# Kernel optimization log

Measured on AMD Instinct MI355X. Metric: run time of the kernel, lower is better.

## Reference

```python
import jax, jax.numpy as jnp
import numpy as np

B, N = 64, 1500
F_MIN, F_MAX = 0.5, 3.0  # HR band in Hz (30-180 bpm)
SAMPLING_F = 0.002       # frequency grid step -> F = 1251 frequencies
FS = 30.0                # video frame rate


def setup_inputs() -> dict:
    key = jax.random.key(0)
    k1, k2 = jax.random.split(key)
    x = jax.random.normal(k1, (B, N), dtype=jnp.float32)
    # true frequencies inside the searched band
    f_true = jax.random.uniform(k2, (B,), dtype=jnp.float32, minval=F_MIN, maxval=F_MAX)
    fs = jnp.full((B,), FS, dtype=jnp.float32)
    deltas = jnp.zeros((B,), dtype=jnp.float32)  # accepted but unused by the loss
    return {
        "x": x,
        "f_true": f_true,
        "fs": fs,
        "deltas": deltas,
        "sampling_f": SAMPLING_F,
        "f_range": (F_MIN, F_MAX),
    }


def reference(x, f_true, fs, deltas, sampling_f, f_range):
    f_min, f_max = f_range
    # frequency grid, same semantics as torch.arange(f_min, f_max+step, step)
    f_values = jnp.arange(f_min, f_max + sampling_f, sampling_f, dtype=jnp.float32)  # [F]
    n = jnp.arange(x.shape[1], dtype=jnp.float32)  # [N] time indices
    # angles[b,f,n] = 2*pi * f_values[f] * n / fs[b]  (fs varies per sample)
    phase = (2.0 * jnp.pi) * (f_values[None, :, None] * n[None, None, :]) / fs[:, None, None]  # [B,F,N]
    # PSD at each grid frequency: (sum x cos)^2 + (sum x sin)^2, batched as one contraction
    cos_terms = jnp.einsum('bn,bfn->bf', x, jnp.cos(phase))  # [B,F]
    sin_terms = jnp.einsum('bn,bfn->bf', x, jnp.sin(phase))  # [B,F]
    psd = cos_terms ** 2 + sin_terms ** 2                    # [B,F]
    log_lik = jnp.log(jax.nn.softmax(psd, axis=1) + 1e-8)    # [B,F]
    # index of grid frequency closest to f_true (non-differentiable gather index)
    idx = jnp.argmin(jnp.abs(f_values[None, :] - f_true[:, None]), axis=1)  # [B]
    per_sample = -jnp.take_along_axis(log_lik, idx[:, None], axis=1)[:, 0]  # [B]
    return jnp.mean(per_sample)
```

## Files before the change

### kernel.cpp

```cpp
#include <hip/hip_runtime.h>

#define BATCH 64
#define NSAMP 1500
#define NFREQ 1251
#define NSEG  5
#define SEGLEN 300
#define FBLK  256
#define FCHUNKS 5


#define CTRL_CNT    0
#define CTRL_GCNT   64
#define CTRL_PROBE  128
#define CTRL_PIDX   256
#define CTRL_LVAL   320
#define CTRL_STATS  384

__device__ __forceinline__ unsigned rmw_read32(unsigned* p) {
    return __hip_atomic_fetch_add(p, 0u, __ATOMIC_RELAXED, __HIP_MEMORY_SCOPE_AGENT);
}
__device__ __forceinline__ unsigned long long rmw_read64(unsigned long long* p) {
    return __hip_atomic_fetch_add(p, 0ull, __ATOMIC_RELAXED, __HIP_MEMORY_SCOPE_AGENT);
}

__global__ __launch_bounds__(256) void fused_kernel(
    const float* __restrict__ x,
    const float* __restrict__ f_true,
    const float* __restrict__ fs,
    const float* __restrict__ sampling_f,
    const float* __restrict__ f_range,
    unsigned* __restrict__ ctrl,
    float* __restrict__ out)
{
    __shared__ float4 xs4[NSAMP / 4];
    __shared__ float red[4], red2[4];
    __shared__ unsigned s_arr;

    const int b      = blockIdx.x;
    const int fchunk = blockIdx.y;
    const int tid    = threadIdx.x;
    const int wave   = tid >> 6;
    const int lane   = tid & 63;

    unsigned long long* stats = (unsigned long long*)(ctrl + CTRL_STATS);

    const float4* xg = reinterpret_cast<const float4*>(x + b * NSAMP);
    for (int i = tid; i < NSAMP / 4; i += FBLK) xs4[i] = xg[i];
    __syncthreads();

    const float f_min = f_range[0];
    const float step  = sampling_f[0];
    const float delta = (f_min + step) - f_min;

    const int  fidx  = fchunk * FBLK + tid;
    const bool valid = (fidx < NFREQ);

    float v = 0.0f;
    if (valid) {
        const float fv  = f_min + (float)fidx * delta;
        const float rho = fv / fs[b];
        float rf = rho - floorf(rho);
        const float coef = 2.0f * __builtin_amdgcn_cosf(rf);

        float s1[NSEG], s2[NSEG];
#pragma unroll
        for (int g = 0; g < NSEG; ++g) { s1[g] = 0.0f; s2[g] = 0.0f; }

#pragma unroll 3
        for (int k = 0; k < SEGLEN / 4; ++k) {
#pragma unroll
            for (int g = 0; g < NSEG; ++g) {
                float4 vv = xs4[g * (SEGLEN / 4) + k];
                float t;
                t = fmaf(coef, s1[g], vv.x - s2[g]); s2[g] = s1[g]; s1[g] = t;
                t = fmaf(coef, s1[g], vv.y - s2[g]); s2[g] = s1[g]; s1[g] = t;
                t = fmaf(coef, s1[g], vv.z - s2[g]); s2[g] = s1[g]; s1[g] = t;
                t = fmaf(coef, s1[g], vv.w - s2[g]); s2[g] = s1[g]; s1[g] = t;
            }
        }

        float aM  = (float)SEGLEN * rho;        aM  -= floorf(aM);
        float aM1 = (float)(SEGLEN - 1) * rho;  aM1 -= floorf(aM1);
        const float cM  = __builtin_amdgcn_cosf(aM);
        const float sM  = __builtin_amdgcn_sinf(aM);
        const float cM1 = __builtin_amdgcn_cosf(aM1);
        const float sM1 = __builtin_amdgcn_sinf(aM1);

        float C = 0.0f, S = 0.0f;
#pragma unroll
        for (int g = 0; g < NSEG; ++g) {
            float a0 = (float)(g * SEGLEN) * rho;  a0 -= floorf(a0);
            const float c0 = __builtin_amdgcn_cosf(a0);
            const float s0 = __builtin_amdgcn_sinf(a0);
            const float Cl = cM1 * s1[g] - cM * s2[g];
            const float Sl = sM1 * s1[g] - sM * s2[g];
            C += c0 * Cl - s0 * Sl;
            S += s0 * Cl + c0 * Sl;
        }
        v = fmaf(C, C, S * S);
    }

    const float ft = f_true[b];
    int iq = (int)((ft - f_min) / delta + 0.5f);
    int lo = iq - 2; if (lo < 0) lo = 0;
    int hi = iq + 2; if (hi > NFREQ - 1) hi = NFREQ - 1;
    int   idx   = lo;
    float bestd = fabsf((f_min + (float)lo * delta) - ft);
    for (int i = lo + 1; i <= hi; ++i) {
        float d = fabsf((f_min + (float)i * delta) - ft);
        if (d < bestd) { bestd = d; idx = i; }
    }
    if (valid && fidx == idx)
        __hip_atomic_exchange(&ctrl[CTRL_PIDX + b], __float_as_uint(v),
                              __ATOMIC_RELAXED, __HIP_MEMORY_SCOPE_AGENT);

    float mt = valid ? v : -INFINITY;
    for (int off = 32; off > 0; off >>= 1) mt = fmaxf(mt, __shfl_xor(mt, off));
    if (lane == 0) red[wave] = mt;
    __syncthreads();
    const float mb = fmaxf(fmaxf(red[0], red[1]), fmaxf(red[2], red[3]));
    float e = valid ? __expf(v - mb) : 0.0f;
    for (int off = 32; off > 0; off >>= 1) e += __shfl_xor(e, off);
    if (lane == 0) red2[wave] = e;
    __syncthreads();
    const float lb = red2[0] + red2[1] + red2[2] + red2[3];

    if (tid == 0) {
        unsigned long long p =
            ((unsigned long long)__float_as_uint(lb) << 32) | __float_as_uint(mb);
        __hip_atomic_exchange(&stats[b * FCHUNKS + fchunk], p,
                              __ATOMIC_RELAXED, __HIP_MEMORY_SCOPE_AGENT);
        const unsigned E = rmw_read32(&ctrl[CTRL_PROBE + b]);
        const unsigned old = __hip_atomic_fetch_add(&ctrl[CTRL_CNT + b], 1u,
                              __ATOMIC_ACQ_REL, __HIP_MEMORY_SCOPE_AGENT);
        s_arr = old - E;
    }
    __syncthreads();
    if (s_arr != FCHUNKS - 1 || tid != 0) return;

    float gm = -INFINITY, gl = 0.0f;
#pragma unroll
    for (int c = 0; c < FCHUNKS; ++c) {
        unsigned long long p = rmw_read64(&stats[b * FCHUNKS + c]);
        const float mc = __uint_as_float((unsigned)p);
        const float lc = __uint_as_float((unsigned)(p >> 32));
        const float mn = fmaxf(gm, mc);
        gl = gl * __expf(gm - mn) + lc * __expf(mc - mn);
        gm = mn;
    }
    const float pv  = __uint_as_float(rmw_read32(&ctrl[CTRL_PIDX + b]));
    const float sm  = __expf(pv - gm) / gl;
    const float per = -logf(sm + 1e-8f);

    __hip_atomic_exchange(&ctrl[CTRL_LVAL + b], __float_as_uint(per),
                          __ATOMIC_RELAXED, __HIP_MEMORY_SCOPE_AGENT);
    const unsigned E2   = rmw_read32(&ctrl[CTRL_PROBE + CTRL_GCNT]);
    const unsigned old2 = __hip_atomic_fetch_add(&ctrl[CTRL_GCNT], 1u,
                          __ATOMIC_ACQ_REL, __HIP_MEMORY_SCOPE_AGENT);
    if (old2 - E2 != BATCH - 1) return;

    float total = 0.0f;
    for (int bb = 0; bb < BATCH; ++bb)
        total += __uint_as_float(rmw_read32(&ctrl[CTRL_LVAL + bb]));
    out[0] = total * (1.0f / (float)BATCH);
}

extern "C" void kernel_launch(void* const* d_in, const int* in_sizes, int n_in,
                              void* d_out, int out_size, void* d_ws, size_t ws_size,
                              hipStream_t stream) {
    const float* x          = (const float*)d_in[0];
    const float* f_true     = (const float*)d_in[1];
    const float* fs         = (const float*)d_in[2];
    const float* sampling_f = (const float*)d_in[4];
    const float* f_range    = (const float*)d_in[5];

    unsigned* ctrl = (unsigned*)((char*)d_ws + (4u << 20));

    dim3 grid(BATCH, FCHUNKS);
    fused_kernel<<<grid, FBLK, 0, stream>>>(x, f_true, fs, sampling_f, f_range,
                                            ctrl, (float*)d_out);
}
```

Before: 87.48 us.

## Split Goertzel recurrence across four thread quarters per frequency and combine in LDS

```diff
diff --git a/kernel.cpp b/kernel.cpp
--- a/kernel.cpp
+++ b/kernel.cpp
@@ -3,10 +3,10 @@
 #define BATCH 64
 #define NSAMP 1500
 #define NFREQ 1251
-#define NSEG  5
-#define SEGLEN 300
 #define FBLK  256
 #define FCHUNKS 5
+#define NQ    4
+#define QSTEP 376
 
 
 #define CTRL_CNT    0
@@ -16,14 +16,7 @@
 #define CTRL_LVAL   320
 #define CTRL_STATS  384
 
-__device__ __forceinline__ unsigned rmw_read32(unsigned* p) {
-    return __hip_atomic_fetch_add(p, 0u, __ATOMIC_RELAXED, __HIP_MEMORY_SCOPE_AGENT);
-}
-__device__ __forceinline__ unsigned long long rmw_read64(unsigned long long* p) {
-    return __hip_atomic_fetch_add(p, 0ull, __ATOMIC_RELAXED, __HIP_MEMORY_SCOPE_AGENT);
-}
-
-__global__ __launch_bounds__(256) void fused_kernel(
+__global__ __launch_bounds__(1024) void fused_kernel(
     const float* __restrict__ x,
     const float* __restrict__ f_true,
     const float* __restrict__ fs,
@@ -33,135 +26,142 @@
     float* __restrict__ out)
 {
     __shared__ float4 xs4[NSAMP / 4];
-    __shared__ float red[4], red2[4];
-    __shared__ unsigned s_arr;
+    __shared__ float2 comb[FBLK * NQ];
+    __shared__ float red[16], red2[16];
 
     const int b      = blockIdx.x;
     const int fchunk = blockIdx.y;
     const int tid    = threadIdx.x;
+    const int q      = tid >> 8;
+    const int f      = tid & 255;
     const int wave   = tid >> 6;
     const int lane   = tid & 63;
 
-    unsigned long long* stats = (unsigned long long*)(ctrl + CTRL_STATS);
-
     const float4* xg = reinterpret_cast<const float4*>(x + b * NSAMP);
-    for (int i = tid; i < NSAMP / 4; i += FBLK) xs4[i] = xg[i];
+    if (tid < NSAMP / 4) xs4[tid] = xg[tid];
     __syncthreads();
 
     const float f_min = f_range[0];
     const float step  = sampling_f[0];
     const float delta = (f_min + step) - f_min;
 
-    const int  fidx  = fchunk * FBLK + tid;
+    const int  fidx  = fchunk * FBLK + f;
     const bool valid = (fidx < NFREQ);
 
-    float v = 0.0f;
-    if (valid) {
+    {
         const float fv  = f_min + (float)fidx * delta;
         const float rho = fv / fs[b];
         float rf = rho - floorf(rho);
         const float coef = 2.0f * __builtin_amdgcn_cosf(rf);
 
-        float s1[NSEG], s2[NSEG];
-#pragma unroll
-        for (int g = 0; g < NSEG; ++g) { s1[g] = 0.0f; s2[g] = 0.0f; }
+        const int n0   = q * QSTEP;
+        const int len  = (q < 3) ? QSTEP : (NSAMP - 3 * QSTEP);
+        const int b4   = n0 >> 2;
+        const int len4 = len >> 2;
 
-#pragma unroll 3
-        for (int k = 0; k < SEGLEN / 4; ++k) {
-#pragma unroll
-            for (int g = 0; g < NSEG; ++g) {
-                float4 vv = xs4[g * (SEGLEN / 4) + k];
-                float t;
-                t = fmaf(coef, s1[g], vv.x - s2[g]); s2[g] = s1[g]; s1[g] = t;
-                t = fmaf(coef, s1[g], vv.y - s2[g]); s2[g] = s1[g]; s1[g] = t;
-                t = fmaf(coef, s1[g], vv.z - s2[g]); s2[g] = s1[g]; s1[g] = t;
-                t = fmaf(coef, s1[g], vv.w - s2[g]); s2[g] = s1[g]; s1[g] = t;
-            }
+        float s1 = 0.0f, s2 = 0.0f;
+#pragma unroll 4
+        for (int k = 0; k < len4; ++k) {
+            float4 v = xs4[b4 + k];
+            float t;
+            t = fmaf(coef, s1, v.x - s2); s2 = s1; s1 = t;
+            t = fmaf(coef, s1, v.y - s2); s2 = s1; s1 = t;
+            t = fmaf(coef, s1, v.z - s2); s2 = s1; s1 = t;
+            t = fmaf(coef, s1, v.w - s2); s2 = s1; s1 = t;
         }
 
-        float aM  = (float)SEGLEN * rho;        aM  -= floorf(aM);
-        float aM1 = (float)(SEGLEN - 1) * rho;  aM1 -= floorf(aM1);
+        float aM  = (float)len * rho;        aM  -= floorf(aM);
+        float aM1 = (float)(len - 1) * rho;  aM1 -= floorf(aM1);
+        float a0  = (float)n0 * rho;         a0  -= floorf(a0);
         const float cM  = __builtin_amdgcn_cosf(aM);
         const float sM  = __builtin_amdgcn_sinf(aM);
         const float cM1 = __builtin_amdgcn_cosf(aM1);
         const float sM1 = __builtin_amdgcn_sinf(aM1);
+        const float c0  = __builtin_amdgcn_cosf(a0);
+        const float s0  = __builtin_amdgcn_sinf(a0);
 
+        const float Cl = cM1 * s1 - cM * s2;
+        const float Sl = sM1 * s1 - sM * s2;
+        comb[f * NQ + q] = make_float2(c0 * Cl - s0 * Sl,
+                                       s0 * Cl + c0 * Sl);
+    }
+    __syncthreads();
+
+    float v = 0.0f;
+    if (q == 0 && valid) {
         float C = 0.0f, S = 0.0f;
 #pragma unroll
-        for (int g = 0; g < NSEG; ++g) {
-            float a0 = (float)(g * SEGLEN) * rho;  a0 -= floorf(a0);
-            const float c0 = __builtin_amdgcn_cosf(a0);
-            const float s0 = __builtin_amdgcn_sinf(a0);
-            const float Cl = cM1 * s1[g] - cM * s2[g];
-            const float Sl = sM1 * s1[g] - sM * s2[g];
-            C += c0 * Cl - s0 * Sl;
-            S += s0 * Cl + c0 * Sl;
+        for (int qq = 0; qq < NQ; ++qq) {
+            float2 p = comb[f * NQ + qq];
+            C += p.x; S += p.y;
         }
         v = fmaf(C, C, S * S);
     }
 
-    const float ft = f_true[b];
-    int iq = (int)((ft - f_min) / delta + 0.5f);
-    int lo = iq - 2; if (lo < 0) lo = 0;
-    int hi = iq + 2; if (hi > NFREQ - 1) hi = NFREQ - 1;
-    int   idx   = lo;
-    float bestd = fabsf((f_min + (float)lo * delta) - ft);
-    for (int i = lo + 1; i <= hi; ++i) {
-        float d = fabsf((f_min + (float)i * delta) - ft);
-        if (d < bestd) { bestd = d; idx = i; }
+    if (q == 0 && valid) {
+        const float ft = f_true[b];
+        int iq2 = (int)((ft - f_min) / delta + 0.5f);
+        int lo = iq2 - 2; if (lo < 0) lo = 0;
+        int hi = iq2 + 2; if (hi > NFREQ - 1) hi = NFREQ - 1;
+        int   idx   = lo;
+        float bestd = fabsf((f_min + (float)lo * delta) - ft);
+        for (int i = lo + 1; i <= hi; ++i) {
+            float d = fabsf((f_min + (float)i * delta) - ft);
+            if (d < bestd) { bestd = d; idx = i; }
+        }
+        if (fidx == idx) ctrl[CTRL_PIDX + b] = __float_as_uint(v);
     }
-    if (valid && fidx == idx)
-        __hip_atomic_exchange(&ctrl[CTRL_PIDX + b], __float_as_uint(v),
-                              __ATOMIC_RELAXED, __HIP_MEMORY_SCOPE_AGENT);
 
-    float mt = valid ? v : -INFINITY;
+    const bool act = (q == 0) && valid;
+    float mt = act ? v : -INFINITY;
     for (int off = 32; off > 0; off >>= 1) mt = fmaxf(mt, __shfl_xor(mt, off));
     if (lane == 0) red[wave] = mt;
     __syncthreads();
-    const float mb = fmaxf(fmaxf(red[0], red[1]), fmaxf(red[2], red[3]));
-    float e = valid ? __expf(v - mb) : 0.0f;
+    float mb = red[0];
+#pragma unroll
+    for (int w = 1; w < 16; ++w) mb = fmaxf(mb, red[w]);
+    float e = act ? __expf(v - mb) : 0.0f;
     for (int off = 32; off > 0; off >>= 1) e += __shfl_xor(e, off);
     if (lane == 0) red2[wave] = e;
     __syncthreads();
-    const float lb = red2[0] + red2[1] + red2[2] + red2[3];
+    float lb = red2[0];
+#pragma unroll
+    for (int w = 1; w < 16; ++w) lb += red2[w];
 
-    if (tid == 0) {
-        unsigned long long p =
-            ((unsigned long long)__float_as_uint(lb) << 32) | __float_as_uint(mb);
-        __hip_atomic_exchange(&stats[b * FCHUNKS + fchunk], p,
-                              __ATOMIC_RELAXED, __HIP_MEMORY_SCOPE_AGENT);
-        const unsigned E = rmw_read32(&ctrl[CTRL_PROBE + b]);
-        const unsigned old = __hip_atomic_fetch_add(&ctrl[CTRL_CNT + b], 1u,
-                              __ATOMIC_ACQ_REL, __HIP_MEMORY_SCOPE_AGENT);
-        s_arr = old - E;
-    }
+    float2* stats = (float2*)(ctrl + CTRL_STATS);
+    if (tid == 0) stats[b * FCHUNKS + fchunk] = make_float2(mb, lb);
+    __threadfence();
     __syncthreads();
-    if (s_arr != FCHUNKS - 1 || tid != 0) return;
+    if (tid != 0) return;
 
+    const unsigned E   = ctrl[CTRL_PROBE + b];
+    const unsigned old = atomicAdd(&ctrl[CTRL_CNT + b], 1u);
+    if (old - E != FCHUNKS - 1) return;
+
+    __threadfence();
     float gm = -INFINITY, gl = 0.0f;
 #pragma unroll
     for (int c = 0; c < FCHUNKS; ++c) {
-        unsigned long long p = rmw_read64(&stats[b * FCHUNKS + c]);
-        const float mc = __uint_as_float((unsigned)p);
-        const float lc = __uint_as_float((unsigned)(p >> 32));
-        const float mn = fmaxf(gm, mc);
-        gl = gl * __expf(gm - mn) + lc * __expf(mc - mn);
+        float2 p = stats[b * FCHUNKS + c];
+        const float mn = fmaxf(gm, p.x);
+        gl = gl * __expf(gm - mn) + p.y * __expf(p.x - mn);
         gm = mn;
     }
-    const float pv  = __uint_as_float(rmw_read32(&ctrl[CTRL_PIDX + b]));
+    const float pv  = __uint_as_float(ctrl[CTRL_PIDX + b]);
     const float sm  = __expf(pv - gm) / gl;
     const float per = -logf(sm + 1e-8f);
 
-    __hip_atomic_exchange(&ctrl[CTRL_LVAL + b], __float_as_uint(per),
-                          __ATOMIC_RELAXED, __HIP_MEMORY_SCOPE_AGENT);
-    const unsigned E2   = rmw_read32(&ctrl[CTRL_PROBE + CTRL_GCNT]);
-    const unsigned old2 = __hip_atomic_fetch_add(&ctrl[CTRL_GCNT], 1u,
-                          __ATOMIC_ACQ_REL, __HIP_MEMORY_SCOPE_AGENT);
+    ctrl[CTRL_LVAL + b] = __float_as_uint(per);
+    __threadfence();
+    const unsigned E2   = ctrl[CTRL_PROBE + CTRL_GCNT];
+    const unsigned old2 = atomicAdd(&ctrl[CTRL_GCNT], 1u);
     if (old2 - E2 != BATCH - 1) return;
 
+    __threadfence();
     float total = 0.0f;
+#pragma unroll 16
     for (int bb = 0; bb < BATCH; ++bb)
-        total += __uint_as_float(rmw_read32(&ctrl[CTRL_LVAL + bb]));
+        total += __uint_as_float(ctrl[CTRL_LVAL + bb]);
     out[0] = total * (1.0f / (float)BATCH);
 }
 
@@ -177,6 +177,6 @@
     unsigned* ctrl = (unsigned*)((char*)d_ws + (4u << 20));
 
     dim3 grid(BATCH, FCHUNKS);
-    fused_kernel<<<grid, FBLK, 0, stream>>>(x, f_true, fs, sampling_f, f_range,
+    fused_kernel<<<grid, 1024, 0, stream>>>(x, f_true, fs, sampling_f, f_range,
                                             ctrl, (float*)d_out);
 }
```

Result: slower. 145.6 us (+66.4%).
